# Performance work log

Measured on AMD Instinct MI355X. Metric: run time of the kernel, lower is better.

## Reference

```python
import jax, jax.numpy as jnp
import numpy as np

B = 2            # batch size
NPB = 49152      # voxels per batch (multiple of GROUP -> padding path is identity)
N = B * NPB
C = 128          # embed_dim
HEADS = 8
GROUP = 128      # group_size
WIN = 12         # win_size
SY, SX = 468, 468  # sparse_shape (y, x)
GD = C // 4      # per-branch channels in CWI_FFN
CONV = WIN + 1   # conv_size = 13


def _bn(x, g, b):
    # training-mode BatchNorm1d, eps=1e-3, biased variance
    m = x.mean(0)
    v = x.var(0)
    return (x - m) * jax.lax.rsqrt(v + 1e-3) * g + b


def _subm_conv(f, w, dense, coords):
    # submanifold sparse 2D conv: output only at active sites, gather active neighbors
    Ky, Kx = w.shape[0], w.shape[1]
    cb, cy, cx = coords[:, 0], coords[:, 1], coords[:, 2]
    out = jnp.zeros((f.shape[0], w.shape[3]), f.dtype)
    for ky in range(Ky):
        for kx in range(Kx):
            ny = cy + (ky - Ky // 2)
            nx = cx + (kx - Kx // 2)
            valid = (ny >= 0) & (ny < SY) & (nx >= 0) & (nx < SX)
            nidx = dense[cb, jnp.clip(ny, 0, SY - 1), jnp.clip(nx, 0, SX - 1)]
            valid = valid & (nidx >= 0)
            nb = jnp.where(valid[:, None], f[jnp.clip(nidx, 0)], 0.0)
            out = out + nb @ w[ky, kx]
    return out


def setup_inputs() -> dict:
    rng = np.random.default_rng(0)
    cs = []
    for b in range(B):
        flat = rng.choice(SY * SX, NPB, replace=False)  # unique voxels per batch
        cs.append(np.stack([np.full(NPB, b), flat // SX, flat % SX], 1))
    coords = jnp.asarray(np.concatenate(cs, 0).astype(np.int32))
    key = jax.random.key(0)
    ks = jax.random.split(key, 10)
    s = lambda k, shape, fan: jax.random.normal(k, shape, jnp.float32) / np.sqrt(fan)
    return dict(
        feats=jax.random.normal(ks[0], (N, C), jnp.float32),
        coords=coords,
        qkv_w=s(ks[1], (C, 3 * C), C),
        fc_out_w=s(ks[2], (C, C), C), fc_out_b=jnp.zeros((C,), jnp.float32),
        norm0_g=jnp.ones((C,), jnp.float32), norm0_b=jnp.zeros((C,), jnp.float32),
        bn1_g=jnp.ones((C,), jnp.float32), bn1_b=jnp.zeros((C,), jnp.float32),
        bn2_g=jnp.ones((C,), jnp.float32), bn2_b=jnp.zeros((C,), jnp.float32),
        convk_w=s(ks[3], (3, 3, GD, GD), 9 * GD),
        convh_w=s(ks[4], (1, CONV, GD, GD), CONV * GD),
        convw_w=s(ks[5], (CONV, 1, GD, GD), CONV * GD),
        fc1_w=s(ks[6], (C, 2 * C), C), fc1_b=jnp.zeros((2 * C,), jnp.float32),
        fc2_w=s(ks[7], (2 * C, C), 2 * C), fc2_b=jnp.zeros((C,), jnp.float32),
    )


def reference(feats, coords, qkv_w, fc_out_w, fc_out_b, norm0_g, norm0_b,
              bn1_g, bn1_b, bn2_g, bn2_b, convk_w, convh_w, convw_w,
              fc1_w, fc1_b, fc2_w, fc2_b):
    # --- FlattenedWindowMapping, direction 'x' (module returns after 1st direction) ---
    mwx = int(np.ceil(SX / WIN)) + 1
    mwy = int(np.ceil(SY / WIN)) + 1
    per = mwx * mwy
    cb = coords[:, 0].astype(jnp.int64)
    cy = coords[:, 1].astype(jnp.int64)
    cx = coords[:, 2].astype(jnp.int64)
    win_id_x = cb * per + (cx // WIN) * mwy + (cy // WIN)
    vx = win_id_x * (WIN * WIN) + (cx % WIN) * WIN + (cy % WIN)  # unique per voxel
    idx = jnp.argsort(vx)
    # counts per batch divide GROUP -> flat2win / win2flat are identity

    # --- grouped multi-head attention ---
    xf = _bn(feats[idx], norm0_g, norm0_b)
    q, k, v = jnp.split(xf @ qkv_w, 3, axis=1)
    ng = N // GROUP
    hd = C // HEADS
    r = lambda t: t.reshape(ng, GROUP, HEADS, hd).transpose(0, 2, 1, 3)  # (n,h,g,d)
    q, k, v = r(q), r(k), r(v)
    att = jax.nn.softmax(jnp.einsum('nhqd,nhkd->nhqk', q, k) / np.sqrt(C), axis=-1)
    out = jnp.einsum('nhqk,nhkd->nhqd', att, v).transpose(0, 2, 1, 3).reshape(N, C)
    out = out @ fc_out_w + fc_out_b
    feats = feats.at[idx].add(out)  # idx is a permutation: residual + scatter-back

    # --- CWI FFN ---
    dense = jnp.full((B, SY, SX), -1, jnp.int32).at[
        coords[:, 0], coords[:, 1], coords[:, 2]].set(jnp.arange(N, dtype=jnp.int32))
    srcn = _bn(feats, bn1_g, bn1_b)
    sk = _subm_conv(srcn[:, :GD], convk_w, dense, coords)
    sh = _subm_conv(srcn[:, GD:2 * GD], convh_w, dense, coords)
    sw = _subm_conv(srcn[:, 2 * GD:3 * GD], convw_w, dense, coords)
    src2 = jnp.concatenate([sk, sh, sw, srcn[:, 3 * GD:]], 1)
    src = srcn + src2
    src2 = jax.nn.relu(_bn(src, bn2_g, bn2_b) @ fc1_w + fc1_b) @ fc2_w + fc2_b
    return src + src2
```

## Files before the change

### kernel.cpp

```cpp
#include <hip/hip_runtime.h>

#define N_PTS 98304
#define SY 468
#define SX 468
#define WIN 12
#define MWY 40
#define PER 1600
#define NWIN 3200
#define NSLOT (NWIN*144)
#define NDENSE (2*SY*SX)
#define CPB 32

using bf16x8 = __attribute__((ext_vector_type(8))) short;
using bf16x4 = __attribute__((ext_vector_type(4))) short;
using f32x4  = __attribute__((ext_vector_type(4))) float;

__device__ __forceinline__ unsigned short f2bf(float f){
  unsigned u = __float_as_uint(f);
  u += 0x7fffu + ((u>>16)&1u);
  return (unsigned short)(u>>16);
}
__device__ __forceinline__ float2 bfp2(unsigned u){
  float2 r; r.x = __uint_as_float(u<<16); r.y = __uint_as_float(u & 0xffff0000u); return r;
}
__device__ __forceinline__ unsigned fpack2(float a, float b){
  return (unsigned)f2bf(a) | ((unsigned)f2bf(b)<<16);
}

__device__ __forceinline__ f32x4 mfma16(bf16x4 a, bf16x4 b, f32x4 c){
#if __has_builtin(__builtin_amdgcn_mfma_f32_16x16x16bf16_1k)
  return __builtin_amdgcn_mfma_f32_16x16x16bf16_1k(a, b, c, 0, 0, 0);
#else
  asm volatile("v_mfma_f32_16x16x16_bf16 %0, %1, %2, %0\n\ts_nop 7\n\ts_nop 7"
               : "+v"(c) : "v"(a), "v"(b));
  return c;
#endif
}

constexpr size_t OFF_SORTED = 0;
constexpr size_t OFF_SLOT   = OFF_SORTED + (size_t)N_PTS*4;
constexpr size_t OFF_CNT    = OFF_SLOT + (size_t)NSLOT*4;
constexpr size_t OFF_OFFS   = OFF_CNT + (size_t)NWIN*4;
constexpr size_t OFF_STATS  = OFF_OFFS + (size_t)NWIN*4;
constexpr size_t OFF_SB     = OFF_STATS + 3*256*4;
constexpr size_t OFF_BQKV   = OFF_SB + 3*256*4;
constexpr size_t OFF_B1     = OFF_BQKV + 512*4;
constexpr size_t OFF_WQKV   = OFF_B1 + 256*4;
constexpr size_t OFF_WOUT   = OFF_WQKV + (size_t)128*384*2;
constexpr size_t OFF_W1     = OFF_WOUT + (size_t)128*128*2;
constexpr size_t OFF_W2     = OFF_W1 + (size_t)128*256*2;
constexpr size_t OFF_WCONV  = OFF_W2 + (size_t)256*128*2;
constexpr size_t OFF_DENSE  = OFF_WCONV + (size_t)35*1024*2;
constexpr size_t OFF_QKV    = (OFF_DENSE + (size_t)NDENSE*4 + 255) & ~(size_t)255;
constexpr size_t OFF_SRC    = OFF_QKV;
constexpr size_t OFF_SRCB   = OFF_QKV + (size_t)N_PTS*128*4;
constexpr size_t OFF_ATT    = OFF_QKV + (size_t)N_PTS*384*2;
constexpr size_t OFF_SRCNB  = OFF_ATT;
constexpr size_t OFF_F2     = OFF_ATT + (size_t)N_PTS*128*2;
constexpr size_t OFF_H      = OFF_F2;
constexpr size_t OFF_SRCNF  = OFF_F2 + (size_t)N_PTS*128*4;

__global__ void fill_i32(int* p, int v, int n){
  int i = blockIdx.x*256 + threadIdx.x;
  if (i < n) p[i] = v;
}

__global__ void keys_kernel(const int* __restrict__ coords, int* __restrict__ slot){
  int i = blockIdx.x*256 + threadIdx.x;
  if (i >= N_PTS) return;
  int cb = coords[3*i], cy = coords[3*i+1], cx = coords[3*i+2];
  int w = cb*PER + (cx/WIN)*MWY + (cy/WIN);
  int sub = (cx%WIN)*WIN + (cy%WIN);
  slot[w*144 + sub] = i;
}

__global__ void wincount_kernel(const int* __restrict__ slot, int* __restrict__ cnt){
  int w = blockIdx.x*256 + threadIdx.x;
  if (w >= NWIN) return;
  int c = 0;
  for (int s = 0; s < 144; ++s) c += (slot[w*144+s] >= 0);
  cnt[w] = c;
}

__global__ void scan_kernel(const int* __restrict__ cnt, int* __restrict__ offs){
  __shared__ int tsum[256];
  int tid = threadIdx.x;
  int loc[13]; int s = 0;
  #pragma unroll
  for (int j = 0; j < 13; ++j){
    int idx = tid*13 + j;
    int v = (idx < NWIN) ? cnt[idx] : 0;
    loc[j] = s; s += v;
  }
  tsum[tid] = s;
  __syncthreads();
  for (int off = 1; off < 256; off <<= 1){
    int v = (tid >= off) ? tsum[tid-off] : 0;
    __syncthreads();
    tsum[tid] += v;
    __syncthreads();
  }
  int pre = (tid > 0) ? tsum[tid-1] : 0;
  #pragma unroll
  for (int j = 0; j < 13; ++j){
    int idx = tid*13 + j;
    if (idx < NWIN) offs[idx] = pre + loc[j];
  }
}

__global__ void scatter_kernel(const int* __restrict__ slot, const int* __restrict__ offs,
                               int* __restrict__ sorted){
  int w = blockIdx.x*256 + threadIdx.x;
  if (w >= NWIN) return;
  int o = offs[w];
  for (int s = 0; s < 144; ++s){
    int v = slot[w*144+s];
    if (v >= 0) sorted[o++] = v;
  }
}

__global__ void dense_kernel(const int* __restrict__ coords, int* __restrict__ dense){
  int i = blockIdx.x*256 + threadIdx.x;
  if (i >= N_PTS) return;
  dense[(coords[3*i]*SY + coords[3*i+1])*SX + coords[3*i+2]] = i;
}

__global__ __launch_bounds__(256) void bnstats_kernel(const float* __restrict__ x, float* __restrict__ stats){
  __shared__ float sh[256], shq[256];
  int tid = threadIdx.x;
  int c = tid & 127;
  float s = 0.f, q = 0.f;
  for (int r = blockIdx.x*2 + (tid>>7); r < N_PTS; r += gridDim.x*2){
    float v = x[(size_t)r*128 + c];
    s += v; q += v*v;
  }
  sh[tid] = s; shq[tid] = q;
  __syncthreads();
  if (tid < 128){
    atomicAdd(&stats[tid],     sh[tid] + sh[tid+128]);
    atomicAdd(&stats[128+tid], shq[tid] + shq[tid+128]);
  }
}

__global__ void bnfinish_kernel(const float* __restrict__ stats, const float* __restrict__ g,
                                const float* __restrict__ b, float* __restrict__ sb){
  int c = threadIdx.x;
  if (c >= 128) return;
  float mean = stats[c] * (1.0f/N_PTS);
  float var  = stats[128+c] * (1.0f/N_PTS) - mean*mean;
  float s = g[c] * rsqrtf(var + 1e-3f);
  sb[c] = s;
  sb[128+c] = b[c] - mean*s;
}

__global__ void packw_kernel(const float* __restrict__ W, const float* __restrict__ scale,
                             short* __restrict__ out, int K, int Nn){
  int t = blockIdx.x*256 + threadIdx.x;
  if (t >= K*Nn) return;
  int e = t & 7, l = (t>>3) & 63, jt = (t>>9) & 7;
  int rest = t >> 12;
  int KT = K >> 5;
  int kt = rest % KT, np = rest / KT;
  int k = kt*32 + ((l>>4)<<3) + e;
  int col = np*128 + jt*16 + (l&15);
  float v = W[(size_t)k*Nn + col];
  if (scale) v *= scale[k];
  out[t] = (short)f2bf(v);
}

__global__ void packbias_kernel(const float* __restrict__ W, const float* __restrict__ bvec,
                                const float* __restrict__ base, float* __restrict__ out, int K, int Nn){
  int o = blockIdx.x*256 + threadIdx.x;
  if (o >= Nn) return;
  float s = base ? base[o] : 0.f;
  for (int k = 0; k < K; ++k) s += bvec[k] * W[(size_t)k*Nn + o];
  out[o] = s;
}

__global__ void packconv_kernel(const float* __restrict__ wk, const float* __restrict__ wh,
                                const float* __restrict__ ww, short* __restrict__ out){
  int t = blockIdx.x*256 + threadIdx.x;
  if (t >= 35*2*64*8) return;
  int e = t & 7, l = (t>>3) & 63, jt = (t>>9) & 1, tap = t >> 10;
  int ci = ((l>>4)<<3) + e;
  int co = jt*16 + (l&15);
  float v;
  if (tap < 9)       v = wk[((size_t)(tap*32) + ci)*32 + co];
  else if (tap < 22) v = wh[((size_t)((tap-9)*32) + ci)*32 + co];
  else               v = ww[((size_t)((tap-22)*32) + ci)*32 + co];
  out[t] = (short)f2bf(v);
}

__global__ __launch_bounds__(256) void srcn_kernel(const float* __restrict__ f2, const float* __restrict__ sb,
                            float* __restrict__ sf, short* __restrict__ sbuf){
  size_t i = (size_t)blockIdx.x*256 + threadIdx.x;
  if (i >= (size_t)N_PTS*32) return;
  int c4 = ((int)(i & 31)) * 4;
  float4 v = ((const float4*)f2)[i];
  float4 o;
  o.x = v.x*sb[c4+0] + sb[128+c4+0];
  o.y = v.y*sb[c4+1] + sb[128+c4+1];
  o.z = v.z*sb[c4+2] + sb[128+c4+2];
  o.w = v.w*sb[c4+3] + sb[128+c4+3];
  ((float4*)sf)[i] = o;
  uint2 h; h.x = fpack2(o.x, o.y); h.y = fpack2(o.z, o.w);
  ((uint2*)sbuf)[i] = h;
}

template<int K, int AMODE, int EPI>
__global__ __launch_bounds__(256) void gemm_kernel(
    const float* __restrict__ Afp, const short* __restrict__ Abf,
    const int* __restrict__ sorted, const short* __restrict__ Wp,
    const float* __restrict__ bias, const float* __restrict__ addf,
    float* __restrict__ outf, short* __restrict__ outb, int dstStride)
{
  extern __shared__ char smem[];
  const int m0 = blockIdx.x * 128;
  const int np = blockIdx.y;
  const int tid = threadIdx.x;
  if (AMODE == 0){
    const int CHK = K/4;
    for (int c = tid; c < 128*CHK; c += 256){
      int r = c / CHK, q = c % CHK;
      const float* arow = Afp + (size_t)sorted[m0+r]*K;
      float4 v = ((const float4*)arow)[q];
      int off = r*(K*2) + q*8; off ^= ((r&7)<<4);
      *reinterpret_cast<uint2*>(smem+off) = make_uint2(fpack2(v.x,v.y), fpack2(v.z,v.w));
    }
  } else {
    const int CHK = K/8;
    for (int c = tid; c < 128*CHK; c += 256){
      int r = c / CHK, q = c % CHK;
      uint4 v = ((const uint4*)(Abf + (size_t)(m0+r)*K))[q];
      int off = r*(K*2) + q*16; off ^= ((r&7)<<4);
      *reinterpret_cast<uint4*>(smem+off) = v;
    }
  }
  __syncthreads();
  const int w = tid >> 6, l = tid & 63, lg = l >> 4, l16 = l & 15;
  f32x4 zacc; zacc[0]=0.f; zacc[1]=0.f; zacc[2]=0.f; zacc[3]=0.f;
  f32x4 acc[2][8];
  #pragma unroll
  for (int mt=0; mt<2; ++mt)
    #pragma unroll
    for (int jt=0; jt<8; ++jt) acc[mt][jt] = zacc;
  const int KT = K/32;
  #pragma unroll
  for (int kt = 0; kt < KT; ++kt){
    const short* wk = Wp + ((size_t)(np*KT + kt))*4096;
    bf16x8 bfr[8];
    #pragma unroll
    for (int jt=0; jt<8; ++jt)
      bfr[jt] = *reinterpret_cast<const bf16x8*>(wk + jt*512 + l*8);
    #pragma unroll
    for (int mt=0; mt<2; ++mt){
      int row = w*32 + mt*16 + l16;
      int off = row*(K*2) + kt*64 + lg*16; off ^= ((row&7)<<4);
      bf16x8 af = *reinterpret_cast<const bf16x8*>(smem + off);
      #pragma unroll
      for (int jt=0; jt<8; ++jt)
        acc[mt][jt] = __builtin_amdgcn_mfma_f32_16x16x32_bf16(af, bfr[jt], acc[mt][jt], 0, 0, 0);
    }
  }
  #pragma unroll
  for (int mt=0; mt<2; ++mt){
    #pragma unroll
    for (int jt=0; jt<8; ++jt){
      int col = np*128 + jt*16 + l16;
      float bv = bias ? bias[col] : 0.f;
      #pragma unroll
      for (int e=0; e<4; ++e){
        int row = m0 + w*32 + mt*16 + lg*4 + e;
        float v = acc[mt][jt][e] + bv;
        if (EPI == 0){
          outb[(size_t)row*dstStride + col] = (short)f2bf(v);
        } else if (EPI == 1){
          int gi = sorted[row];
          outf[(size_t)gi*128 + col] = addf[(size_t)gi*128 + col] + v;
        } else if (EPI == 2){
          outb[(size_t)row*dstStride + col] = (short)f2bf(fmaxf(v, 0.f));
        } else {
          outf[(size_t)row*128 + col] = addf[(size_t)row*128 + col] + v;
        }
      }
    }
  }
}

__global__ __launch_bounds__(256) void attn_kernel(const short* __restrict__ qkv, short* __restrict__ attout){
  __shared__ char VT[32768];
  const int g = blockIdx.x;
  const int tid = threadIdx.x;
  for (int c = tid; c < 128*16; c += 256){
    int r = c >> 4, q = c & 15;
    uint4 v = *(const uint4*)(qkv + ((size_t)(g*128 + r))*384 + 256 + q*8);
    const unsigned short* hv = (const unsigned short*)&v;
    #pragma unroll
    for (int j = 0; j < 8; ++j){
      int cc = q*8 + j;
      int F = ((cc & 7) ^ ((cc >> 3) & 7)) << 4;
      *(unsigned short*)(VT + cc*256 + ((r*2) ^ F)) = hv[j];
    }
  }
  __syncthreads();
  const int w = tid>>6, l = tid&63, lg = l>>4, l16 = l&15;
  const float sc2 = 0.12751744f;
  f32x4 z4; z4[0]=0.f; z4[1]=0.f; z4[2]=0.f; z4[3]=0.f;
  const short* qbase = qkv + (size_t)(g*128)*384;
  for (int h = 0; h < 8; ++h){
    const int ch = h*16 + lg*4;
    bf16x4 qf0 = *(const bf16x4*)(qbase + (size_t)(w*32 + l16)*384 + ch);
    bf16x4 qf1 = *(const bf16x4*)(qbase + (size_t)(w*32 + 16 + l16)*384 + ch);
    f32x4 s[8][2];
    #pragma unroll
    for (int kb=0; kb<8; ++kb){ s[kb][0] = z4; s[kb][1] = z4; }
    #pragma unroll
    for (int kb=0; kb<8; ++kb){
      bf16x4 kf = *(const bf16x4*)(qbase + (size_t)(kb*16 + l16)*384 + 128 + ch);
      s[kb][0] = mfma16(kf, qf0, s[kb][0]);
      s[kb][1] = mfma16(kf, qf1, s[kb][1]);
    }
    float inv0, inv1;
    #pragma unroll
    for (int mt=0; mt<2; ++mt){
      float m = -1e30f;
      #pragma unroll
      for (int kb=0; kb<8; ++kb)
        #pragma unroll
        for (int e=0; e<4; ++e) m = fmaxf(m, s[kb][mt][e]);
      m = fmaxf(m, __shfl_xor(m, 16));
      m = fmaxf(m, __shfl_xor(m, 32));
      float d = 0.f;
      #pragma unroll
      for (int kb=0; kb<8; ++kb)
        #pragma unroll
        for (int e=0; e<4; ++e){
          float p = exp2f((s[kb][mt][e] - m) * sc2);
          s[kb][mt][e] = p; d += p;
        }
      d += __shfl_xor(d, 16);
      d += __shfl_xor(d, 32);
      if (mt == 0) inv0 = 1.0f/d; else inv1 = 1.0f/d;
    }
    f32x4 o0 = z4, o1 = z4;
    const int cc = h*16 + l16;
    const int F = ((cc & 7) ^ ((cc >> 3) & 7)) << 4;
    #pragma unroll
    for (int kb=0; kb<8; ++kb){
      bf16x4 vb = *(const bf16x4*)(VT + cc*256 + ((kb*32 + lg*8) ^ F));
      bf16x4 pa0, pa1;
      #pragma unroll
      for (int e=0; e<4; ++e){
        pa0[e] = (short)f2bf(s[kb][0][e] * inv0);
        pa1[e] = (short)f2bf(s[kb][1][e] * inv1);
      }
      o0 = mfma16(pa0, vb, o0);
      o1 = mfma16(pa1, vb, o1);
    }
    #pragma unroll
    for (int e=0; e<4; ++e){
      int row0 = g*128 + w*32      + lg*4 + e;
      int row1 = g*128 + w*32 + 16 + lg*4 + e;
      attout[(size_t)row0*128 + h*16 + l16] = (short)f2bf(o0[e]);
      attout[(size_t)row1*128 + h*16 + l16] = (short)f2bf(o1[e]);
    }
  }
}

template<int G>
__global__ __launch_bounds__(256) void conv_kernel(
    const short* __restrict__ wfrag, const short* __restrict__ srcnb,
    const float* __restrict__ srcnf, const int* __restrict__ dense,
    const int* __restrict__ coords, float* __restrict__ src)
{
  constexpr int TC   = (G==0) ? 9 : 13;
  constexpr int TAP0 = (G==0) ? 0 : ((G==1) ? 9 : 22);
  __shared__ int scoords[CPB*3];
  __shared__ int nid[CPB*16];
  extern __shared__ char nbf[];
  const int tid = threadIdx.x;
  const int p0 = blockIdx.x * CPB;
  if (tid < CPB*3) scoords[tid] = coords[p0*3 + tid];
  const int w = tid>>6, l = tid&63, lg = l>>4, l16 = l&15;
  const int mt = w & 1, jt = w >> 1;
  bf16x8 bw[TC];
  #pragma unroll
  for (int t = 0; t < TC; ++t)
    bw[t] = *reinterpret_cast<const bf16x8*>(wfrag + (((TAP0+t)*2 + jt)*64 + l)*8);
  __syncthreads();
  for (int i = tid; i < TC*CPB; i += 256){
    int tap = i >> 5, p = i & 31;
    int cb = scoords[p*3], cy = scoords[p*3+1], cx = scoords[p*3+2];
    int dy, dx;
    if (G==0){ dy = tap/3 - 1; dx = tap%3 - 1; }
    else if (G==1){ dy = 0; dx = tap - 6; }
    else { dy = tap - 6; dx = 0; }
    int ny = cy+dy, nx = cx+dx;
    int v = -1;
    if (ny>=0 && ny<SY && nx>=0 && nx<SX) v = dense[(cb*SY+ny)*SX + nx];
    nid[p*16 + tap] = v;
  }
  __syncthreads();
  for (int i = tid; i < TC*CPB*4; i += 256){
    int c = i & 3, s = i >> 2;
    int tap = s >> 5, p = s & 31;
    int v = nid[p*16 + tap];
    uint4 val = make_uint4(0,0,0,0);
    if (v >= 0) val = *(const uint4*)(srcnb + (size_t)v*128 + G*32 + c*8);
    int off = (tap*CPB + p)*80 + ((c*16) ^ ((p&3)<<4));
    *(uint4*)(nbf + off) = val;
  }
  __syncthreads();
  f32x4 acc; acc[0]=0.f; acc[1]=0.f; acc[2]=0.f; acc[3]=0.f;
  const int pA = mt*16 + l16;
  #pragma unroll
  for (int t = 0; t < TC; ++t){
    int off = (t*CPB + pA)*80 + ((lg*16) ^ ((pA&3)<<4));
    bf16x8 af = *reinterpret_cast<const bf16x8*>(nbf + off);
    acc = __builtin_amdgcn_mfma_f32_16x16x32_bf16(af, bw[t], acc, 0, 0, 0);
  }
  #pragma unroll
  for (int e = 0; e < 4; ++e){
    int pi = p0 + mt*16 + lg*4 + e;
    int c = G*32 + jt*16 + l16;
    src[(size_t)pi*128 + c] = srcnf[(size_t)pi*128 + c] + acc[e];
  }
}

__global__ __launch_bounds__(256) void post_kernel(float* __restrict__ src, const float* __restrict__ srcnf,
                           short* __restrict__ srcb, float* __restrict__ stats){
  __shared__ float ss[128], sq[128];
  int tid = threadIdx.x;
  if (tid < 128){ ss[tid]=0.f; sq[tid]=0.f; }
  __syncthreads();
  int c4 = (tid & 31) * 4;
  float a0=0,a1=0,a2=0,a3=0, q0=0,q1=0,q2=0,q3=0;
  for (int r = blockIdx.x*8 + (tid>>5); r < N_PTS; r += gridDim.x*8){
    size_t base = (size_t)r*128 + c4;
    float4 v;
    if (c4 < 96){
      v = *(const float4*)(src + base);
    } else {
      float4 sn = *(const float4*)(srcnf + base);
      v = make_float4(2.f*sn.x, 2.f*sn.y, 2.f*sn.z, 2.f*sn.w);
      *(float4*)(src + base) = v;
    }
    uint2 h; h.x = fpack2(v.x, v.y); h.y = fpack2(v.z, v.w);
    *(uint2*)(srcb + base) = h;
    a0+=v.x; a1+=v.y; a2+=v.z; a3+=v.w;
    q0+=v.x*v.x; q1+=v.y*v.y; q2+=v.z*v.z; q3+=v.w*v.w;
  }
  atomicAdd(&ss[c4+0],a0); atomicAdd(&ss[c4+1],a1); atomicAdd(&ss[c4+2],a2); atomicAdd(&ss[c4+3],a3);
  atomicAdd(&sq[c4+0],q0); atomicAdd(&sq[c4+1],q1); atomicAdd(&sq[c4+2],q2); atomicAdd(&sq[c4+3],q3);
  __syncthreads();
  if (tid < 128){
    atomicAdd(&stats[tid],     ss[tid]);
    atomicAdd(&stats[128+tid], sq[tid]);
  }
}

extern "C" void kernel_launch(void* const* d_in, const int* in_sizes, int n_in,
                              void* d_out, int out_size, void* d_ws, size_t ws_size,
                              hipStream_t stream)
{
  const float* feats    = (const float*)d_in[0];
  const int*   coords   = (const int*)d_in[1];
  const float* qkv_w    = (const float*)d_in[2];
  const float* fc_out_w = (const float*)d_in[3];
  const float* fc_out_b = (const float*)d_in[4];
  const float* norm0_g  = (const float*)d_in[5];
  const float* norm0_b  = (const float*)d_in[6];
  const float* bn1_g    = (const float*)d_in[7];
  const float* bn1_b    = (const float*)d_in[8];
  const float* bn2_g    = (const float*)d_in[9];
  const float* bn2_b    = (const float*)d_in[10];
  const float* convk_w  = (const float*)d_in[11];
  const float* convh_w  = (const float*)d_in[12];
  const float* convw_w  = (const float*)d_in[13];
  const float* fc1_w    = (const float*)d_in[14];
  const float* fc1_b    = (const float*)d_in[15];
  const float* fc2_w    = (const float*)d_in[16];
  const float* fc2_b    = (const float*)d_in[17];
  float* out = (float*)d_out;
  char* ws = (char*)d_ws;

  int*   sorted = (int*)(ws + OFF_SORTED);
  int*   slot   = (int*)(ws + OFF_SLOT);
  int*   cnt    = (int*)(ws + OFF_CNT);
  int*   offs   = (int*)(ws + OFF_OFFS);
  float* stats0 = (float*)(ws + OFF_STATS);
  float* stats1 = stats0 + 256;
  float* stats2 = stats0 + 512;
  float* sb0    = (float*)(ws + OFF_SB);
  float* sb1    = sb0 + 256;
  float* sb2    = sb0 + 512;
  float* bqkv   = (float*)(ws + OFF_BQKV);
  float* b1     = (float*)(ws + OFF_B1);
  short* wqkv   = (short*)(ws + OFF_WQKV);
  short* wout   = (short*)(ws + OFF_WOUT);
  short* w1     = (short*)(ws + OFF_W1);
  short* w2     = (short*)(ws + OFF_W2);
  short* wconv  = (short*)(ws + OFF_WCONV);
  int*   dense  = (int*)(ws + OFF_DENSE);
  short* qkvb   = (short*)(ws + OFF_QKV);
  float* srcf   = (float*)(ws + OFF_SRC);
  short* srcb   = (short*)(ws + OFF_SRCB);
  short* att    = (short*)(ws + OFF_ATT);
  short* srcnb  = (short*)(ws + OFF_SRCNB);
  float* feats2 = (float*)(ws + OFF_F2);
  short* Hbuf   = (short*)(ws + OFF_H);
  float* srcnf  = (float*)(ws + OFF_SRCNF);

  fill_i32<<<(NSLOT+255)/256, 256, 0, stream>>>(slot, -1, NSLOT);
  fill_i32<<<(NDENSE+255)/256, 256, 0, stream>>>(dense, -1, NDENSE);
  fill_i32<<<3, 256, 0, stream>>>((int*)stats0, 0, 768);

  keys_kernel<<<(N_PTS+255)/256, 256, 0, stream>>>(coords, slot);
  wincount_kernel<<<(NWIN+255)/256, 256, 0, stream>>>(slot, cnt);
  scan_kernel<<<1, 256, 0, stream>>>(cnt, offs);
  scatter_kernel<<<(NWIN+255)/256, 256, 0, stream>>>(slot, offs, sorted);
  dense_kernel<<<(N_PTS+255)/256, 256, 0, stream>>>(coords, dense);

  bnstats_kernel<<<512, 256, 0, stream>>>(feats, stats0);
  bnfinish_kernel<<<1, 128, 0, stream>>>(stats0, norm0_g, norm0_b, sb0);
  packw_kernel<<<(128*384+255)/256, 256, 0, stream>>>(qkv_w, sb0, wqkv, 128, 384);
  packbias_kernel<<<2, 256, 0, stream>>>(qkv_w, sb0+128, nullptr, bqkv, 128, 384);
  packw_kernel<<<(128*128+255)/256, 256, 0, stream>>>(fc_out_w, nullptr, wout, 128, 128);

  gemm_kernel<128,0,0><<<dim3(768,3), 256, 32768, stream>>>(feats, nullptr, sorted, wqkv, bqkv, nullptr, nullptr, qkvb, 384);
  attn_kernel<<<768, 256, 0, stream>>>(qkvb, att);
  gemm_kernel<128,1,1><<<dim3(768,1), 256, 32768, stream>>>(nullptr, att, sorted, wout, fc_out_b, feats, feats2, nullptr, 128);

  bnstats_kernel<<<512, 256, 0, stream>>>(feats2, stats1);
  bnfinish_kernel<<<1, 128, 0, stream>>>(stats1, bn1_g, bn1_b, sb1);
  srcn_kernel<<<(N_PTS*32+255)/256, 256, 0, stream>>>(feats2, sb1, srcnf, srcnb);

  packconv_kernel<<<(35*2*64*8+255)/256, 256, 0, stream>>>(convk_w, convh_w, convw_w, wconv);
  conv_kernel<0><<<N_PTS/CPB, 256,  9*CPB*80, stream>>>(wconv, srcnb, srcnf, dense, coords, srcf);
  conv_kernel<1><<<N_PTS/CPB, 256, 13*CPB*80, stream>>>(wconv, srcnb, srcnf, dense, coords, srcf);
  conv_kernel<2><<<N_PTS/CPB, 256, 13*CPB*80, stream>>>(wconv, srcnb, srcnf, dense, coords, srcf);
  post_kernel<<<512, 256, 0, stream>>>(srcf, srcnf, srcb, stats2);
  bnfinish_kernel<<<1, 128, 0, stream>>>(stats2, bn2_g, bn2_b, sb2);

  packw_kernel<<<(128*256+255)/256, 256, 0, stream>>>(fc1_w, sb2, w1, 128, 256);
  packbias_kernel<<<1, 256, 0, stream>>>(fc1_w, sb2+128, fc1_b, b1, 128, 256);
  packw_kernel<<<(256*128+255)/256, 256, 0, stream>>>(fc2_w, nullptr, w2, 256, 128);

  gemm_kernel<128,1,2><<<dim3(768,2), 256, 32768, stream>>>(nullptr, srcb, nullptr, w1, b1, nullptr, nullptr, Hbuf, 256);
  gemm_kernel<256,1,3><<<dim3(768,1), 256, 65536, stream>>>(nullptr, Hbuf, nullptr, w2, fc2_b, srcf, out, nullptr, 128);

  (void)in_sizes; (void)n_in; (void)out_size; (void)ws_size;
}
```

Measured before the change: 646.9 us.

## Fuse BN1 stats into out-proj GEMM, head-blocked QKV layout, drop fp32 srcn

The out-projection GEMM epilogue now accumulates the per-channel sum and sum of squares, reduced in shared memory and then atomically, so the separate bnstats pass over feats2 is gone. The QKV GEMM writes Q/K/V in a per-group, per-head blocked layout, and attention is split across a second grid dimension (two heads per block) with a smaller V-transpose buffer. The fp32 copy of the normalized source is no longer stored; conv and post kernels rebuild the residual from the bf16 copy. This saves memory traffic and a launch, at the cost of bf16 rounding in the residual path and atomic contention on the stats.

```diff
diff --git a/kernel.cpp b/kernel.cpp
--- a/kernel.cpp
+++ b/kernel.cpp
@@ -58,7 +58,6 @@
 constexpr size_t OFF_SRCNB  = OFF_ATT;
 constexpr size_t OFF_F2     = OFF_ATT + (size_t)N_PTS*128*2;
 constexpr size_t OFF_H      = OFF_F2;
-constexpr size_t OFF_SRCNF  = OFF_F2 + (size_t)N_PTS*128*4;
 
 __global__ void fill_i32(int* p, int v, int n){
   int i = blockIdx.x*256 + threadIdx.x;
@@ -192,7 +191,7 @@
 }
 
 __global__ __launch_bounds__(256) void srcn_kernel(const float* __restrict__ f2, const float* __restrict__ sb,
-                            float* __restrict__ sf, short* __restrict__ sbuf){
+                            short* __restrict__ sbuf){
   size_t i = (size_t)blockIdx.x*256 + threadIdx.x;
   if (i >= (size_t)N_PTS*32) return;
   int c4 = ((int)(i & 31)) * 4;
@@ -202,7 +201,6 @@
   o.y = v.y*sb[c4+1] + sb[128+c4+1];
   o.z = v.z*sb[c4+2] + sb[128+c4+2];
   o.w = v.w*sb[c4+3] + sb[128+c4+3];
-  ((float4*)sf)[i] = o;
   uint2 h; h.x = fpack2(o.x, o.y); h.y = fpack2(o.z, o.w);
   ((uint2*)sbuf)[i] = h;
 }
@@ -212,7 +210,8 @@
     const float* __restrict__ Afp, const short* __restrict__ Abf,
     const int* __restrict__ sorted, const short* __restrict__ Wp,
     const float* __restrict__ bias, const float* __restrict__ addf,
-    float* __restrict__ outf, short* __restrict__ outb, int dstStride)
+    float* __restrict__ outf, short* __restrict__ outb, float* __restrict__ stats,
+    int dstStride)
 {
   extern __shared__ char smem[];
   const int m0 = blockIdx.x * 128;
@@ -262,6 +261,9 @@
         acc[mt][jt] = __builtin_amdgcn_mfma_f32_16x16x32_bf16(af, bfr[jt], acc[mt][jt], 0, 0, 0);
     }
   }
+  float psum[8], psq[8];
+  #pragma unroll
+  for (int jt=0; jt<8; ++jt){ psum[jt]=0.f; psq[jt]=0.f; }
   #pragma unroll
   for (int mt=0; mt<2; ++mt){
     #pragma unroll
@@ -276,47 +278,74 @@
           outb[(size_t)row*dstStride + col] = (short)f2bf(v);
         } else if (EPI == 1){
           int gi = sorted[row];
-          outf[(size_t)gi*128 + col] = addf[(size_t)gi*128 + col] + v;
+          float fv = addf[(size_t)gi*128 + col] + v;
+          outf[(size_t)gi*128 + col] = fv;
+          psum[jt] += fv; psq[jt] += fv*fv;
         } else if (EPI == 2){
           outb[(size_t)row*dstStride + col] = (short)f2bf(fmaxf(v, 0.f));
+        } else if (EPI == 3){
+          outf[(size_t)row*128 + col] = addf[(size_t)row*128 + col] + v;
         } else {
-          outf[(size_t)row*128 + col] = addf[(size_t)row*128 + col] + v;
+          int r = row - m0;
+          int blk = (m0 >> 7)*24 + np*8 + jt;
+          outb[(size_t)blk*2048 + r*16 + l16] = (short)f2bf(v);
         }
       }
     }
   }
+  if (EPI == 1){
+    __syncthreads();
+    float* cs = (float*)smem;
+    cs[tid] = 0.f;
+    __syncthreads();
+    float* cq = cs + 128;
+    #pragma unroll
+    for (int jt=0; jt<8; ++jt){
+      atomicAdd(&cs[jt*16 + l16], psum[jt]);
+      atomicAdd(&cq[jt*16 + l16], psq[jt]);
+    }
+    __syncthreads();
+    if (tid < 128){
+      atomicAdd(&stats[tid],     cs[tid]);
+      atomicAdd(&stats[128+tid], cq[tid]);
+    }
+  }
 }
 
 __global__ __launch_bounds__(256) void attn_kernel(const short* __restrict__ qkv, short* __restrict__ attout){
-  __shared__ char VT[32768];
+  __shared__ char VT[8192];
   const int g = blockIdx.x;
+  const int hp = blockIdx.y;
   const int tid = threadIdx.x;
-  for (int c = tid; c < 128*16; c += 256){
-    int r = c >> 4, q = c & 15;
-    uint4 v = *(const uint4*)(qkv + ((size_t)(g*128 + r))*384 + 256 + q*8);
+  const short* gb = qkv + (size_t)g*24*2048;
+  for (int c = tid; c < 512; c += 256){
+    int hh = c >> 8, idx = c & 255, token = idx >> 1, q = idx & 1;
+    uint4 v = *(const uint4*)(gb + (16 + 2*hp + hh)*2048 + token*16 + q*8);
     const unsigned short* hv = (const unsigned short*)&v;
     #pragma unroll
     for (int j = 0; j < 8; ++j){
-      int cc = q*8 + j;
-      int F = ((cc & 7) ^ ((cc >> 3) & 7)) << 4;
-      *(unsigned short*)(VT + cc*256 + ((r*2) ^ F)) = hv[j];
+      int ch = hh*16 + q*8 + j;
+      int F = ((ch & 7) ^ ((ch >> 3) & 7)) << 4;
+      *(unsigned short*)(VT + ch*256 + ((token*2) ^ F)) = hv[j];
     }
   }
   __syncthreads();
   const int w = tid>>6, l = tid&63, lg = l>>4, l16 = l&15;
   const float sc2 = 0.12751744f;
   f32x4 z4; z4[0]=0.f; z4[1]=0.f; z4[2]=0.f; z4[3]=0.f;
-  const short* qbase = qkv + (size_t)(g*128)*384;
-  for (int h = 0; h < 8; ++h){
-    const int ch = h*16 + lg*4;
-    bf16x4 qf0 = *(const bf16x4*)(qbase + (size_t)(w*32 + l16)*384 + ch);
-    bf16x4 qf1 = *(const bf16x4*)(qbase + (size_t)(w*32 + 16 + l16)*384 + ch);
+  #pragma unroll
+  for (int hh = 0; hh < 2; ++hh){
+    const int h = 2*hp + hh;
+    const short* Qb = gb + h*2048;
+    const short* Kb = gb + (8 + h)*2048;
+    bf16x4 qf0 = *(const bf16x4*)(Qb + (w*32      + l16)*16 + lg*4);
+    bf16x4 qf1 = *(const bf16x4*)(Qb + (w*32 + 16 + l16)*16 + lg*4);
     f32x4 s[8][2];
     #pragma unroll
     for (int kb=0; kb<8; ++kb){ s[kb][0] = z4; s[kb][1] = z4; }
     #pragma unroll
     for (int kb=0; kb<8; ++kb){
-      bf16x4 kf = *(const bf16x4*)(qbase + (size_t)(kb*16 + l16)*384 + 128 + ch);
+      bf16x4 kf = *(const bf16x4*)(Kb + (kb*16 + l16)*16 + lg*4);
       s[kb][0] = mfma16(kf, qf0, s[kb][0]);
       s[kb][1] = mfma16(kf, qf1, s[kb][1]);
     }
@@ -343,7 +372,7 @@
       if (mt == 0) inv0 = 1.0f/d; else inv1 = 1.0f/d;
     }
     f32x4 o0 = z4, o1 = z4;
-    const int cc = h*16 + l16;
+    const int cc = hh*16 + l16;
     const int F = ((cc & 7) ^ ((cc >> 3) & 7)) << 4;
     #pragma unroll
     for (int kb=0; kb<8; ++kb){
@@ -370,8 +399,8 @@
 template<int G>
 __global__ __launch_bounds__(256) void conv_kernel(
     const short* __restrict__ wfrag, const short* __restrict__ srcnb,
-    const float* __restrict__ srcnf, const int* __restrict__ dense,
-    const int* __restrict__ coords, float* __restrict__ src)
+    const int* __restrict__ dense, const int* __restrict__ coords,
+    float* __restrict__ src)
 {
   constexpr int TC   = (G==0) ? 9 : 13;
   constexpr int TAP0 = (G==0) ? 0 : ((G==1) ? 9 : 22);
@@ -423,11 +452,12 @@
   for (int e = 0; e < 4; ++e){
     int pi = p0 + mt*16 + lg*4 + e;
     int c = G*32 + jt*16 + l16;
-    src[(size_t)pi*128 + c] = srcnf[(size_t)pi*128 + c] + acc[e];
-  }
-}
-
-__global__ __launch_bounds__(256) void post_kernel(float* __restrict__ src, const float* __restrict__ srcnf,
+    unsigned short rv = ((const unsigned short*)srcnb)[(size_t)pi*128 + c];
+    src[(size_t)pi*128 + c] = __uint_as_float((unsigned)rv << 16) + acc[e];
+  }
+}
+
+__global__ __launch_bounds__(256) void post_kernel(float* __restrict__ src, const short* __restrict__ srcnb,
                            short* __restrict__ srcb, float* __restrict__ stats){
   __shared__ float ss[128], sq[128];
   int tid = threadIdx.x;
@@ -441,8 +471,9 @@
     if (c4 < 96){
       v = *(const float4*)(src + base);
     } else {
-      float4 sn = *(const float4*)(srcnf + base);
-      v = make_float4(2.f*sn.x, 2.f*sn.y, 2.f*sn.z, 2.f*sn.w);
+      uint2 sn = *(const uint2*)(srcnb + base);
+      float2 p0 = bfp2(sn.x), p1 = bfp2(sn.y);
+      v = make_float4(2.f*p0.x, 2.f*p0.y, 2.f*p1.x, 2.f*p1.y);
       *(float4*)(src + base) = v;
     }
     uint2 h; h.x = fpack2(v.x, v.y); h.y = fpack2(v.z, v.w);
@@ -509,7 +540,6 @@
   short* srcnb  = (short*)(ws + OFF_SRCNB);
   float* feats2 = (float*)(ws + OFF_F2);
   short* Hbuf   = (short*)(ws + OFF_H);
-  float* srcnf  = (float*)(ws + OFF_SRCNF);
 
   fill_i32<<<(NSLOT+255)/256, 256, 0, stream>>>(slot, -1, NSLOT);
   fill_i32<<<(NDENSE+255)/256, 256, 0, stream>>>(dense, -1, NDENSE);
@@ -527,27 +557,26 @@
   packbias_kernel<<<2, 256, 0, stream>>>(qkv_w, sb0+128, nullptr, bqkv, 128, 384);
   packw_kernel<<<(128*128+255)/256, 256, 0, stream>>>(fc_out_w, nullptr, wout, 128, 128);
 
-  gemm_kernel<128,0,0><<<dim3(768,3), 256, 32768, stream>>>(feats, nullptr, sorted, wqkv, bqkv, nullptr, nullptr, qkvb, 384);
-  attn_kernel<<<768, 256, 0, stream>>>(qkvb, att);
-  gemm_kernel<128,1,1><<<dim3(768,1), 256, 32768, stream>>>(nullptr, att, sorted, wout, fc_out_b, feats, feats2, nullptr, 128);
-
-  bnstats_kernel<<<512, 256, 0, stream>>>(feats2, stats1);
+  gemm_kernel<128,0,4><<<dim3(768,3), 256, 32768, stream>>>(feats, nullptr, sorted, wqkv, bqkv, nullptr, nullptr, qkvb, nullptr, 0);
+  attn_kernel<<<dim3(768,4), 256, 0, stream>>>(qkvb, att);
+  gemm_kernel<128,1,1><<<dim3(768,1), 256, 32768, stream>>>(nullptr, att, sorted, wout, fc_out_b, feats, feats2, nullptr, stats1, 128);
+
   bnfinish_kernel<<<1, 128, 0, stream>>>(stats1, bn1_g, bn1_b, sb1);
-  srcn_kernel<<<(N_PTS*32+255)/256, 256, 0, stream>>>(feats2, sb1, srcnf, srcnb);
+  srcn_kernel<<<(N_PTS*32+255)/256, 256, 0, stream>>>(feats2, sb1, srcnb);
 
   packconv_kernel<<<(35*2*64*8+255)/256, 256, 0, stream>>>(convk_w, convh_w, convw_w, wconv);
-  conv_kernel<0><<<N_PTS/CPB, 256,  9*CPB*80, stream>>>(wconv, srcnb, srcnf, dense, coords, srcf);
-  conv_kernel<1><<<N_PTS/CPB, 256, 13*CPB*80, stream>>>(wconv, srcnb, srcnf, dense, coords, srcf);
-  conv_kernel<2><<<N_PTS/CPB, 256, 13*CPB*80, stream>>>(wconv, srcnb, srcnf, dense, coords, srcf);
-  post_kernel<<<512, 256, 0, stream>>>(srcf, srcnf, srcb, stats2);
+  conv_kernel<0><<<N_PTS/CPB, 256,  9*CPB*80, stream>>>(wconv, srcnb, dense, coords, srcf);
+  conv_kernel<1><<<N_PTS/CPB, 256, 13*CPB*80, stream>>>(wconv, srcnb, dense, coords, srcf);
+  conv_kernel<2><<<N_PTS/CPB, 256, 13*CPB*80, stream>>>(wconv, srcnb, dense, coords, srcf);
+  post_kernel<<<512, 256, 0, stream>>>(srcf, srcnb, srcb, stats2);
   bnfinish_kernel<<<1, 128, 0, stream>>>(stats2, bn2_g, bn2_b, sb2);
 
   packw_kernel<<<(128*256+255)/256, 256, 0, stream>>>(fc1_w, sb2, w1, 128, 256);
   packbias_kernel<<<1, 256, 0, stream>>>(fc1_w, sb2+128, fc1_b, b1, 128, 256);
   packw_kernel<<<(256*128+255)/256, 256, 0, stream>>>(fc2_w, nullptr, w2, 256, 128);
 
-  gemm_kernel<128,1,2><<<dim3(768,2), 256, 32768, stream>>>(nullptr, srcb, nullptr, w1, b1, nullptr, nullptr, Hbuf, 256);
-  gemm_kernel<256,1,3><<<dim3(768,1), 256, 65536, stream>>>(nullptr, Hbuf, nullptr, w2, fc2_b, srcf, out, nullptr, 128);
+  gemm_kernel<128,1,2><<<dim3(768,2), 256, 32768, stream>>>(nullptr, srcb, nullptr, w1, b1, nullptr, nullptr, Hbuf, nullptr, 256);
+  gemm_kernel<256,1,3><<<dim3(768,1), 256, 65536, stream>>>(nullptr, Hbuf, nullptr, w2, fc2_b, srcf, out, nullptr, nullptr, 128);
 
   (void)in_sizes; (void)n_in; (void)out_size; (void)ws_size;
 }
```

Measured after the change: 611.8 us. 5.4% less time.
